# Performance work log

Measured on AMD Instinct MI355X. Metric: run time of the kernel, lower is better.

Reference implementation:

```python
import jax, jax.numpy as jnp
import numpy as np

P_PARTS = 6
NUM_CLASSES = 50000
BATCH = 128
PART_DIM = 256
LABEL_SMOOTH = 0.1
MARGIN = 0.3
TEMP = 3.0
KL_CLAMP = 5.0
LAMBDA_GRAPH = 0.1
LAMBDA_TRI = 1.0
LAMBDA_ADV = 0.1
START_EPOCH = 20


def setup_inputs() -> dict:
    key = jax.random.key(0)
    ks = jax.random.split(key, 8)
    id_logits = jax.random.normal(ks[0], (P_PARTS, BATCH, NUM_CLASSES), dtype=jnp.float32)
    id_features = jax.random.normal(ks[1], (P_PARTS, BATCH, PART_DIM), dtype=jnp.float32)
    gray_features = jax.random.normal(ks[2], (P_PARTS, BATCH, PART_DIM), dtype=jnp.float32)
    # soft labels are probability distributions (teacher softmax outputs)
    soft_labels = jax.nn.softmax(jax.random.normal(ks[3], (P_PARTS, BATCH, NUM_CLASSES), dtype=jnp.float32), axis=-1)
    entropy_weights = jax.random.uniform(ks[4], (P_PARTS, BATCH), dtype=jnp.float32)
    adv_logits = jax.random.normal(ks[5], (P_PARTS, BATCH, 2), dtype=jnp.float32)
    labels = jax.random.randint(ks[6], (BATCH,), 0, 16, dtype=jnp.int64 if jax.config.jax_enable_x64 else jnp.int32)
    modality_labels = jax.random.randint(ks[7], (BATCH,), 0, 2, dtype=jnp.int64 if jax.config.jax_enable_x64 else jnp.int32)
    return {
        'id_logits': id_logits,
        'id_features': id_features,
        'gray_features': gray_features,
        'soft_labels': soft_labels,
        'entropy_weights': entropy_weights,
        'adv_logits': adv_logits,
        'labels': labels,
        'modality_labels': modality_labels,
        'current_epoch': 25,
    }


def _ce(logits, labels, smoothing):
    # torch CrossEntropyLoss with label_smoothing, mean reduction. logits: [B,C]
    logp = jax.nn.log_softmax(logits, axis=-1)
    nll = -jnp.take_along_axis(logp, labels[:, None], axis=-1)[:, 0]
    smooth = -jnp.mean(logp, axis=-1)
    return jnp.mean((1.0 - smoothing) * nll + smoothing * smooth)


def _triplet(feat, target_feat, labels, same):
    # euclidean cdist [B,B]
    sq = (jnp.sum(feat * feat, axis=1)[:, None]
          + jnp.sum(target_feat * target_feat, axis=1)[None, :]
          - 2.0 * feat @ target_feat.T)
    dist = jnp.sqrt(jnp.clip(sq, 0.0) + 1e-12)
    eq = labels[:, None] == labels[None, :]
    is_neg = ~eq
    is_pos = eq & (~jnp.eye(feat.shape[0], dtype=bool)) if same else eq
    # vectorized hard mining (replaces per-row python loop)
    dist_ap = jnp.where(is_pos.any(axis=1),
                        jnp.max(jnp.where(is_pos, dist, -jnp.inf), axis=1), 0.0)
    dist_an = jnp.where(is_neg.any(axis=1),
                        jnp.min(jnp.where(is_neg, dist, jnp.inf), axis=1), 1e6)
    # MarginRankingLoss with y=1: mean(relu(dist_ap - dist_an + margin))
    return jnp.mean(jnp.maximum(dist_ap - dist_an + MARGIN, 0.0))


def reference(id_logits, id_features, gray_features, soft_labels, entropy_weights,
              adv_logits, labels, modality_labels, current_epoch):
    P = id_logits.shape[0]
    # --- multi-part ID loss ---
    L_id = jnp.mean(jax.vmap(lambda lg: _ce(lg, labels, LABEL_SMOOTH))(id_logits))
    # --- triplet on L2-normalized concatenated part features ---
    feat = jnp.concatenate(list(id_features), axis=1)  # [B, P*D]
    feat = feat / jnp.linalg.norm(feat, axis=1, keepdims=True)
    L_tri = _triplet(feat, feat, labels, same=True)
    feat_gray = jnp.concatenate(list(gray_features), axis=1)
    feat_gray = feat_gray / jnp.linalg.norm(feat_gray, axis=1, keepdims=True)
    L_trans = _triplet(feat, feat_gray, labels, same=False)
    L_tri = L_tri + 0.5 * L_trans
    # --- graph distillation (KL) ---
    if current_epoch >= START_EPOCH:
        logp = jax.nn.log_softmax(id_logits / TEMP, axis=-1)  # [P,B,C]
        kl = jnp.sum(soft_labels * (jnp.log(soft_labels) - logp), axis=-1)  # [P,B]
        kl = jnp.minimum(kl, KL_CLAMP)
        L_graph = jnp.sum(jnp.mean(kl * entropy_weights, axis=1)) * (TEMP ** 2) / P
    else:
        L_graph = jnp.float32(0.0)
    # --- adversarial CE ---
    logp_adv = jax.nn.log_softmax(adv_logits, axis=-1)  # [P,B,2]
    nll_adv = -jnp.take_along_axis(logp_adv, modality_labels[None, :, None], axis=-1)[..., 0]
    L_adv = jnp.mean(jnp.mean(nll_adv, axis=1))
    total = L_id + LAMBDA_TRI * L_tri + LAMBDA_GRAPH * L_graph + LAMBDA_ADV * L_adv
    return total
```

## Files before the change

### kernel.cpp

```cpp
#include <hip/hip_runtime.h>

#define NCLS   50000
#define NC4    12500
#define BATCH  128
#define PPARTS 6
#define NROWS  768
#define FD     1536

__device__ __forceinline__ float wave_sum(float v) {
#pragma unroll
  for (int off = 32; off > 0; off >>= 1) v += __shfl_xor(v, off, 64);
  return v;
}

__global__ void zero_k(float* acc) {
  if (threadIdx.x < 8) acc[threadIdx.x] = 0.0f;
}

__global__ __launch_bounds__(256) void big_rows_k(
    const float* __restrict__ X, const float* __restrict__ S,
    const float* __restrict__ W, const int* __restrict__ labels,
    float* __restrict__ acc) {
  const int row = blockIdx.x;
  const int b = row & (BATCH - 1);
  const int t = threadIdx.x;
  const size_t base = (size_t)row * NCLS;
  const float4* x4 = (const float4*)(X + base);
  const float4* s4 = (const float4*)(S + base);
  const float i3 = 1.0f / 3.0f;

  float x_lab = 0.0f;
  if (t == 0) x_lab = X[base + labels[b]];

  float m = -1e30f, e1 = 0.0f, e2 = 0.0f;
  float sx = 0.0f, ss = 0.0f, ssl = 0.0f, ssx = 0.0f;

  for (int i = t; i < NC4; i += 256) {
    float4 xv = x4[i];
    float4 sv = s4[i];
    float xs[4] = {xv.x, xv.y, xv.z, xv.w};
    float sc[4] = {sv.x, sv.y, sv.z, sv.w};
#pragma unroll
    for (int c = 0; c < 4; ++c) {
      float x = xs[c], s = sc[c];
      if (x > m) {
        float d = m - x;
        e1 *= __expf(d);
        e2 *= __expf(d * i3);
        m = x;
      }
      float d = x - m;
      e1 += __expf(d);
      e2 += __expf(d * i3);
      sx += x;
      ss += s;
      ssl = fmaf(s, __logf(s), ssl);
      ssx = fmaf(s, x, ssx);
    }
  }

#pragma unroll
  for (int off = 32; off > 0; off >>= 1) {
    float mo  = __shfl_xor(m, off, 64);
    float e1o = __shfl_xor(e1, off, 64);
    float e2o = __shfl_xor(e2, off, 64);
    float nm = fmaxf(m, mo);
    e1 = e1 * __expf(m - nm) + e1o * __expf(mo - nm);
    e2 = e2 * __expf((m - nm) * i3) + e2o * __expf((mo - nm) * i3);
    m = nm;
    sx  += __shfl_xor(sx, off, 64);
    ss  += __shfl_xor(ss, off, 64);
    ssl += __shfl_xor(ssl, off, 64);
    ssx += __shfl_xor(ssx, off, 64);
  }

  __shared__ float rm[4], re1[4], re2[4], rsx[4], rss[4], rssl[4], rssx[4];
  const int lane = t & 63, wid = t >> 6;
  if (lane == 0) {
    rm[wid] = m; re1[wid] = e1; re2[wid] = e2;
    rsx[wid] = sx; rss[wid] = ss; rssl[wid] = ssl; rssx[wid] = ssx;
  }
  __syncthreads();
  if (t == 0) {
    float M = rm[0], E1 = re1[0], E2 = re2[0];
#pragma unroll
    for (int wv = 1; wv < 4; ++wv) {
      float nm = fmaxf(M, rm[wv]);
      E1 = E1 * __expf(M - nm) + re1[wv] * __expf(rm[wv] - nm);
      E2 = E2 * __expf((M - nm) * i3) + re2[wv] * __expf((rm[wv] - nm) * i3);
      M = nm;
    }
    float SX  = rsx[0] + rsx[1] + rsx[2] + rsx[3];
    float SS  = rss[0] + rss[1] + rss[2] + rss[3];
    float SSL = rssl[0] + rssl[1] + rssl[2] + rssl[3];
    float SSX = rssx[0] + rssx[1] + rssx[2] + rssx[3];
    float logZ  = M + __logf(E1);
    float logZT = M * i3 + __logf(E2);
    float ce = 0.9f * (logZ - x_lab) + 0.1f * (logZ - SX * (1.0f / NCLS));
    float kl = SSL - SSX * i3 + logZT * SS;
    kl = fminf(kl, 5.0f);
    atomicAdd(&acc[0], ce);
    atomicAdd(&acc[1], kl * W[row]);
  }
}

__global__ __launch_bounds__(256) void normalize_k(
    const float* __restrict__ idf, const float* __restrict__ grayf,
    float* __restrict__ Fn, float* __restrict__ Gn) {
  const int src = blockIdx.x >> 7;
  const int b = blockIdx.x & (BATCH - 1);
  const int t = threadIdx.x;
  const float* in = src ? grayf : idf;
  float* out = src ? Gn : Fn;

  float v[6];
  float sq = 0.0f;
#pragma unroll
  for (int k = 0; k < 6; ++k) {
    v[k] = in[((k * BATCH + b) << 8) + t];
    sq = fmaf(v[k], v[k], sq);
  }
  sq = wave_sum(sq);
  __shared__ float wsum[4];
  __shared__ float inv_s;
  const int lane = t & 63, wid = t >> 6;
  if (lane == 0) wsum[wid] = sq;
  __syncthreads();
  if (t == 0) inv_s = 1.0f / sqrtf(wsum[0] + wsum[1] + wsum[2] + wsum[3]);
  __syncthreads();
  float inv = inv_s;
#pragma unroll
  for (int k = 0; k < 6; ++k)
    out[b * FD + (k << 8) + t] = v[k] * inv;
}

__global__ __launch_bounds__(256) void dist_k(
    const float* __restrict__ Fn, const float* __restrict__ Gn,
    float* __restrict__ D) {
  const int z = blockIdx.z;
  const float* Bm = z ? Gn : Fn;
  const int i0 = blockIdx.y * 16, j0 = blockIdx.x * 16;
  const int tx = threadIdx.x, ty = threadIdx.y;
  __shared__ float As[16][17], Bs[16][17];
  float acc = 0.0f;
  for (int k0 = 0; k0 < FD; k0 += 16) {
    As[ty][tx] = Fn[(i0 + ty) * FD + k0 + tx];
    Bs[ty][tx] = Bm[(j0 + ty) * FD + k0 + tx];
    __syncthreads();
#pragma unroll
    for (int k = 0; k < 16; ++k) acc = fmaf(As[ty][k], Bs[tx][k], acc);
    __syncthreads();
  }
  float sq = fmaxf(2.0f - 2.0f * acc, 0.0f) + 1e-12f;
  D[z * BATCH * BATCH + (i0 + ty) * BATCH + j0 + tx] = sqrtf(sq);
}

__global__ void mine_k(const float* __restrict__ D,
                       const int* __restrict__ labels, float* __restrict__ acc) {
  const int b = threadIdx.x;
  __shared__ int slab[BATCH];
  slab[b] = labels[b];
  __syncthreads();
  const int lb = slab[b];
  const float* d1 = D + b * BATCH;
  const float* d2 = D + BATCH * BATCH + b * BATCH;
  float ap1 = -1e30f, an1 = 1e30f, ap2 = -1e30f, an2 = 1e30f;
  int hasp1 = 0, hasn = 0, hasp2 = 0;
  for (int j = 0; j < BATCH; ++j) {
    bool eq = (slab[j] == lb);
    float v1 = d1[j], v2 = d2[j];
    if (eq) {
      hasp2 = 1; ap2 = fmaxf(ap2, v2);
      if (j != b) { hasp1 = 1; ap1 = fmaxf(ap1, v1); }
    } else {
      hasn = 1; an1 = fminf(an1, v1); an2 = fminf(an2, v2);
    }
  }
  float dap1 = hasp1 ? ap1 : 0.0f;
  float dan1 = hasn ? an1 : 1e6f;
  float l1 = fmaxf(dap1 - dan1 + 0.3f, 0.0f);
  float dap2 = hasp2 ? ap2 : 0.0f;
  float dan2 = hasn ? an2 : 1e6f;
  float l2 = fmaxf(dap2 - dan2 + 0.3f, 0.0f);
  l1 = wave_sum(l1);
  l2 = wave_sum(l2);
  __shared__ float r1[2], r2[2];
  const int lane = b & 63, wid = b >> 6;
  if (lane == 0) { r1[wid] = l1; r2[wid] = l2; }
  __syncthreads();
  if (b == 0) { acc[2] = r1[0] + r1[1]; acc[3] = r2[0] + r2[1]; }
}

__global__ void adv_k(const float* __restrict__ advl,
                      const int* __restrict__ mod, float* __restrict__ acc) {
  const int t = threadIdx.x;
  float sum = 0.0f;
#pragma unroll
  for (int k = 0; k < 3; ++k) {
    int r = t + k * 256;
    int b = r & (BATCH - 1);
    float l0 = advl[2 * r], l1 = advl[2 * r + 1];
    float mx = fmaxf(l0, l1);
    float lse = mx + __logf(__expf(l0 - mx) + __expf(l1 - mx));
    sum += lse - (mod[b] ? l1 : l0);
  }
  sum = wave_sum(sum);
  __shared__ float rs[4];
  const int lane = t & 63, wid = t >> 6;
  if (lane == 0) rs[wid] = sum;
  __syncthreads();
  if (t == 0) acc[4] = rs[0] + rs[1] + rs[2] + rs[3];
}

__global__ void fin_k(const float* __restrict__ acc,
                      const int* __restrict__ epoch, float* __restrict__ out) {
  float L_id = acc[0] * (1.0f / NROWS);
  float L_tri = acc[2] * (1.0f / BATCH) + 0.5f * acc[3] * (1.0f / BATCH);
  float L_graph = (epoch[0] >= 20) ? acc[1] * (9.0f / (6.0f * BATCH)) : 0.0f;
  float L_adv = acc[4] * (1.0f / NROWS);
  out[0] = L_id + 1.0f * L_tri + 0.1f * L_graph + 0.1f * L_adv;
}

extern "C" void kernel_launch(void* const* d_in, const int* in_sizes, int n_in,
                              void* d_out, int out_size, void* d_ws, size_t ws_size,
                              hipStream_t stream) {
  (void)in_sizes; (void)n_in; (void)out_size; (void)ws_size;
  const float* id_logits = (const float*)d_in[0];
  const float* id_feat   = (const float*)d_in[1];
  const float* gray_feat = (const float*)d_in[2];
  const float* soft      = (const float*)d_in[3];
  const float* entw      = (const float*)d_in[4];
  const float* advl      = (const float*)d_in[5];
  const int*   labels    = (const int*)d_in[6];
  const int*   modality  = (const int*)d_in[7];
  const int*   epoch     = (const int*)d_in[8];
  float* out = (float*)d_out;

  float* acc = (float*)d_ws;
  float* Fn  = acc + 16;
  float* Gn  = Fn + BATCH * FD;
  float* D   = Gn + BATCH * FD;

  zero_k<<<1, 64, 0, stream>>>(acc);
  big_rows_k<<<NROWS, 256, 0, stream>>>(id_logits, soft, entw, labels, acc);
  normalize_k<<<256, 256, 0, stream>>>(id_feat, gray_feat, Fn, Gn);
  dist_k<<<dim3(8, 8, 2), dim3(16, 16), 0, stream>>>(Fn, Gn, D);
  mine_k<<<1, BATCH, 0, stream>>>(D, labels, acc);
  adv_k<<<1, 256, 0, stream>>>(advl, modality, acc);
  fin_k<<<1, 1, 0, stream>>>(acc, epoch, out);
}
```

Baseline: 407.8 us.

## Restructure loss pipeline: fewer launches, chunked online softmax, fused tail kernel

The big row-reduction kernel now runs 512 threads per row and processes each float4 as a chunk, taking one max and one rescale per four elements instead of a per-element branch. Normalization now stores only inverse norms, which the distance GEMM applies directly to the raw features using 32x32 tiles with a 2x2 register block. Mining, the adversarial CE and finalization are fused into one tail kernel, and the accumulator zeroing moves into the norm kernel, cutting the launch count from seven to four. The main cost targeted is the memory-bound 768-row pass plus per-launch overhead; the risk is lower occupancy or register pressure at 512 threads.

```diff
diff --git a/kernel.cpp b/kernel.cpp
--- a/kernel.cpp
+++ b/kernel.cpp
@@ -13,11 +13,31 @@
   return v;
 }
 
-__global__ void zero_k(float* acc) {
-  if (threadIdx.x < 8) acc[threadIdx.x] = 0.0f;
-}
-
-__global__ __launch_bounds__(256) void big_rows_k(
+#define WS_INVF 16
+#define WS_INVG 144
+#define WS_D    272
+
+__device__ __forceinline__ void chunk_update(float4 xv, float4 sv,
+    float& m, float& e1, float& e2, float& sx, float& ss, float& ssl, float& ssx) {
+  const float i3 = 1.0f / 3.0f;
+  float cm = fmaxf(fmaxf(xv.x, xv.y), fmaxf(xv.z, xv.w));
+  float nm = fmaxf(m, cm);
+  float d0 = xv.x - nm, d1 = xv.y - nm, d2 = xv.z - nm, d3 = xv.w - nm;
+  float r = m - nm;
+  e1 = fmaf(e1, __expf(r),
+            (__expf(d0) + __expf(d1)) + (__expf(d2) + __expf(d3)));
+  e2 = fmaf(e2, __expf(r * i3),
+            (__expf(d0 * i3) + __expf(d1 * i3)) + (__expf(d2 * i3) + __expf(d3 * i3)));
+  m = nm;
+  sx += (xv.x + xv.y) + (xv.z + xv.w);
+  ss += (sv.x + sv.y) + (sv.z + sv.w);
+  ssl = fmaf(sv.x, __logf(sv.x), fmaf(sv.y, __logf(sv.y),
+        fmaf(sv.z, __logf(sv.z), fmaf(sv.w, __logf(sv.w), ssl))));
+  ssx = fmaf(sv.x, xv.x, fmaf(sv.y, xv.y,
+        fmaf(sv.z, xv.z, fmaf(sv.w, xv.w, ssx))));
+}
+
+__global__ __launch_bounds__(512) void big_rows_k(
     const float* __restrict__ X, const float* __restrict__ S,
     const float* __restrict__ W, const int* __restrict__ labels,
     float* __restrict__ acc) {
@@ -29,34 +49,19 @@
   const float4* s4 = (const float4*)(S + base);
   const float i3 = 1.0f / 3.0f;
 
-  float x_lab = 0.0f;
-  if (t == 0) x_lab = X[base + labels[b]];
+  float x_lab = (t == 0) ? X[base + labels[b]] : 0.0f;
 
   float m = -1e30f, e1 = 0.0f, e2 = 0.0f;
   float sx = 0.0f, ss = 0.0f, ssl = 0.0f, ssx = 0.0f;
 
-  for (int i = t; i < NC4; i += 256) {
-    float4 xv = x4[i];
-    float4 sv = s4[i];
-    float xs[4] = {xv.x, xv.y, xv.z, xv.w};
-    float sc[4] = {sv.x, sv.y, sv.z, sv.w};
-#pragma unroll
-    for (int c = 0; c < 4; ++c) {
-      float x = xs[c], s = sc[c];
-      if (x > m) {
-        float d = m - x;
-        e1 *= __expf(d);
-        e2 *= __expf(d * i3);
-        m = x;
-      }
-      float d = x - m;
-      e1 += __expf(d);
-      e2 += __expf(d * i3);
-      sx += x;
-      ss += s;
-      ssl = fmaf(s, __logf(s), ssl);
-      ssx = fmaf(s, x, ssx);
-    }
+#pragma unroll 4
+  for (int k = 0; k < 24; ++k) {
+    int i = t + (k << 9);
+    chunk_update(x4[i], s4[i], m, e1, e2, sx, ss, ssl, ssx);
+  }
+  {
+    int i = 12288 + t;
+    if (i < NC4) chunk_update(x4[i], s4[i], m, e1, e2, sx, ss, ssl, ssx);
   }
 
 #pragma unroll
@@ -74,7 +79,7 @@
     ssx += __shfl_xor(ssx, off, 64);
   }
 
-  __shared__ float rm[4], re1[4], re2[4], rsx[4], rss[4], rssl[4], rssx[4];
+  __shared__ float rm[8], re1[8], re2[8], rsx[8], rss[8], rssl[8], rssx[8];
   const int lane = t & 63, wid = t >> 6;
   if (lane == 0) {
     rm[wid] = m; re1[wid] = e1; re2[wid] = e2;
@@ -84,16 +89,15 @@
   if (t == 0) {
     float M = rm[0], E1 = re1[0], E2 = re2[0];
 #pragma unroll
-    for (int wv = 1; wv < 4; ++wv) {
+    for (int wv = 1; wv < 8; ++wv) {
       float nm = fmaxf(M, rm[wv]);
       E1 = E1 * __expf(M - nm) + re1[wv] * __expf(rm[wv] - nm);
       E2 = E2 * __expf((M - nm) * i3) + re2[wv] * __expf((rm[wv] - nm) * i3);
       M = nm;
     }
-    float SX  = rsx[0] + rsx[1] + rsx[2] + rsx[3];
-    float SS  = rss[0] + rss[1] + rss[2] + rss[3];
-    float SSL = rssl[0] + rssl[1] + rssl[2] + rssl[3];
-    float SSX = rssx[0] + rssx[1] + rssx[2] + rssx[3];
+    float SX = 0.f, SS = 0.f, SSL = 0.f, SSX = 0.f;
+#pragma unroll
+    for (int wv = 0; wv < 8; ++wv) { SX += rsx[wv]; SS += rss[wv]; SSL += rssl[wv]; SSX += rssx[wv]; }
     float logZ  = M + __logf(E1);
     float logZT = M * i3 + __logf(E2);
     float ce = 0.9f * (logZ - x_lab) + 0.1f * (logZ - SX * (1.0f / NCLS));
@@ -104,121 +108,129 @@
   }
 }
 
-__global__ __launch_bounds__(256) void normalize_k(
+__global__ __launch_bounds__(256) void norm_k(
     const float* __restrict__ idf, const float* __restrict__ grayf,
-    float* __restrict__ Fn, float* __restrict__ Gn) {
+    float* __restrict__ ws) {
   const int src = blockIdx.x >> 7;
   const int b = blockIdx.x & (BATCH - 1);
   const int t = threadIdx.x;
   const float* in = src ? grayf : idf;
-  float* out = src ? Gn : Fn;
-
-  float v[6];
   float sq = 0.0f;
 #pragma unroll
   for (int k = 0; k < 6; ++k) {
-    v[k] = in[((k * BATCH + b) << 8) + t];
-    sq = fmaf(v[k], v[k], sq);
+    float v = in[((k * BATCH + b) << 8) + t];
+    sq = fmaf(v, v, sq);
   }
   sq = wave_sum(sq);
-  __shared__ float wsum[4];
-  __shared__ float inv_s;
+  __shared__ float w4[4];
   const int lane = t & 63, wid = t >> 6;
-  if (lane == 0) wsum[wid] = sq;
-  __syncthreads();
-  if (t == 0) inv_s = 1.0f / sqrtf(wsum[0] + wsum[1] + wsum[2] + wsum[3]);
-  __syncthreads();
-  float inv = inv_s;
-#pragma unroll
-  for (int k = 0; k < 6; ++k)
-    out[b * FD + (k << 8) + t] = v[k] * inv;
+  if (lane == 0) w4[wid] = sq;
+  __syncthreads();
+  if (t == 0)
+    ws[16 + src * BATCH + b] = 1.0f / sqrtf(w4[0] + w4[1] + w4[2] + w4[3]);
+  if (blockIdx.x == 0 && t < 16) ws[t] = 0.0f;
 }
 
 __global__ __launch_bounds__(256) void dist_k(
-    const float* __restrict__ Fn, const float* __restrict__ Gn,
-    float* __restrict__ D) {
+    const float* __restrict__ idf, const float* __restrict__ grayf,
+    float* __restrict__ ws) {
   const int z = blockIdx.z;
-  const float* Bm = z ? Gn : Fn;
-  const int i0 = blockIdx.y * 16, j0 = blockIdx.x * 16;
-  const int tx = threadIdx.x, ty = threadIdx.y;
-  __shared__ float As[16][17], Bs[16][17];
-  float acc = 0.0f;
-  for (int k0 = 0; k0 < FD; k0 += 16) {
-    As[ty][tx] = Fn[(i0 + ty) * FD + k0 + tx];
-    Bs[ty][tx] = Bm[(j0 + ty) * FD + k0 + tx];
+  const float* Bm = z ? grayf : idf;
+  const float* invJsrc = ws + (z ? WS_INVG : WS_INVF);
+  const float* invIsrc = ws + WS_INVF;
+  float* D = ws + WS_D + z * BATCH * BATCH;
+  const int i0 = blockIdx.y * 32, j0 = blockIdx.x * 32;
+  const int t = threadIdx.x;
+
+  __shared__ float As[32][33], Bs[32][33];
+  __shared__ float sInvI[32], sInvJ[32];
+  if (t < 32) sInvI[t] = invIsrc[i0 + t];
+  else if (t < 64) sInvJ[t - 32] = invJsrc[j0 + t - 32];
+
+  const int lr = t >> 3, lk = (t & 7) << 2;
+  const int ty = t >> 4, tx = t & 15;
+
+  float c00 = 0.f, c01 = 0.f, c10 = 0.f, c11 = 0.f;
+  for (int k0 = 0; k0 < FD; k0 += 32) {
+    const int p = (k0 + lk) >> 8;
+    const int kin = (k0 + lk) & 255;
+    float4 av = *(const float4*)&idf[((p * BATCH + i0 + lr) << 8) + kin];
+    float4 bv = *(const float4*)&Bm [((p * BATCH + j0 + lr) << 8) + kin];
+    As[lr][lk] = av.x; As[lr][lk+1] = av.y; As[lr][lk+2] = av.z; As[lr][lk+3] = av.w;
+    Bs[lr][lk] = bv.x; Bs[lr][lk+1] = bv.y; Bs[lr][lk+2] = bv.z; Bs[lr][lk+3] = bv.w;
     __syncthreads();
 #pragma unroll
-    for (int k = 0; k < 16; ++k) acc = fmaf(As[ty][k], Bs[tx][k], acc);
+    for (int k = 0; k < 32; ++k) {
+      float a0 = As[2*ty][k],   a1 = As[2*ty+1][k];
+      float b0 = Bs[2*tx][k],   b1 = Bs[2*tx+1][k];
+      c00 = fmaf(a0, b0, c00);  c01 = fmaf(a0, b1, c01);
+      c10 = fmaf(a1, b0, c10);  c11 = fmaf(a1, b1, c11);
+    }
     __syncthreads();
   }
-  float sq = fmaxf(2.0f - 2.0f * acc, 0.0f) + 1e-12f;
-  D[z * BATCH * BATCH + (i0 + ty) * BATCH + j0 + tx] = sqrtf(sq);
-}
-
-__global__ void mine_k(const float* __restrict__ D,
-                       const int* __restrict__ labels, float* __restrict__ acc) {
-  const int b = threadIdx.x;
+  float ii0 = sInvI[2*ty], ii1 = sInvI[2*ty+1];
+  float jj0 = sInvJ[2*tx], jj1 = sInvJ[2*tx+1];
+  float g00 = c00*ii0*jj0, g01 = c01*ii0*jj1, g10 = c10*ii1*jj0, g11 = c11*ii1*jj1;
+  D[(i0+2*ty  )*BATCH + j0+2*tx  ] = sqrtf(fmaxf(2.f-2.f*g00, 0.f) + 1e-12f);
+  D[(i0+2*ty  )*BATCH + j0+2*tx+1] = sqrtf(fmaxf(2.f-2.f*g01, 0.f) + 1e-12f);
+  D[(i0+2*ty+1)*BATCH + j0+2*tx  ] = sqrtf(fmaxf(2.f-2.f*g10, 0.f) + 1e-12f);
+  D[(i0+2*ty+1)*BATCH + j0+2*tx+1] = sqrtf(fmaxf(2.f-2.f*g11, 0.f) + 1e-12f);
+}
+
+__global__ __launch_bounds__(256) void tail_k(
+    const float* __restrict__ ws_c, const float* __restrict__ advl,
+    const int* __restrict__ labels, const int* __restrict__ mod,
+    const int* __restrict__ epoch, float* __restrict__ out) {
+  const int t = threadIdx.x;
   __shared__ int slab[BATCH];
-  slab[b] = labels[b];
-  __syncthreads();
+  __shared__ float red[8];
+  if (t < BATCH) slab[t] = labels[t];
+  __syncthreads();
+
+  const int z = t >> 7;
+  const int b = t & (BATCH - 1);
   const int lb = slab[b];
-  const float* d1 = D + b * BATCH;
-  const float* d2 = D + BATCH * BATCH + b * BATCH;
-  float ap1 = -1e30f, an1 = 1e30f, ap2 = -1e30f, an2 = 1e30f;
-  int hasp1 = 0, hasn = 0, hasp2 = 0;
+  const float* drow = ws_c + WS_D + z * BATCH * BATCH + b * BATCH;
+  float ap = -1e30f, an = 1e30f;
+  int hasp = 0, hasn = 0;
+#pragma unroll 4
   for (int j = 0; j < BATCH; ++j) {
     bool eq = (slab[j] == lb);
-    float v1 = d1[j], v2 = d2[j];
-    if (eq) {
-      hasp2 = 1; ap2 = fmaxf(ap2, v2);
-      if (j != b) { hasp1 = 1; ap1 = fmaxf(ap1, v1); }
-    } else {
-      hasn = 1; an1 = fminf(an1, v1); an2 = fminf(an2, v2);
-    }
-  }
-  float dap1 = hasp1 ? ap1 : 0.0f;
-  float dan1 = hasn ? an1 : 1e6f;
-  float l1 = fmaxf(dap1 - dan1 + 0.3f, 0.0f);
-  float dap2 = hasp2 ? ap2 : 0.0f;
-  float dan2 = hasn ? an2 : 1e6f;
-  float l2 = fmaxf(dap2 - dan2 + 0.3f, 0.0f);
-  l1 = wave_sum(l1);
-  l2 = wave_sum(l2);
-  __shared__ float r1[2], r2[2];
-  const int lane = b & 63, wid = b >> 6;
-  if (lane == 0) { r1[wid] = l1; r2[wid] = l2; }
-  __syncthreads();
-  if (b == 0) { acc[2] = r1[0] + r1[1]; acc[3] = r2[0] + r2[1]; }
-}
-
-__global__ void adv_k(const float* __restrict__ advl,
-                      const int* __restrict__ mod, float* __restrict__ acc) {
-  const int t = threadIdx.x;
-  float sum = 0.0f;
+    float v = drow[j];
+    bool posok = eq && (z == 1 || j != b);
+    if (posok) { hasp = 1; ap = fmaxf(ap, v); }
+    if (!eq)   { hasn = 1; an = fminf(an, v); }
+  }
+  float dap = hasp ? ap : 0.0f;
+  float dan = hasn ? an : 1e6f;
+  float hinge = fmaxf(dap - dan + 0.3f, 0.0f);
+  hinge = wave_sum(hinge);
+
+  float advs = 0.0f;
 #pragma unroll
   for (int k = 0; k < 3; ++k) {
-    int r = t + k * 256;
-    int b = r & (BATCH - 1);
+    int r = t + (k << 8);
+    int rb = r & (BATCH - 1);
     float l0 = advl[2 * r], l1 = advl[2 * r + 1];
     float mx = fmaxf(l0, l1);
     float lse = mx + __logf(__expf(l0 - mx) + __expf(l1 - mx));
-    sum += lse - (mod[b] ? l1 : l0);
-  }
-  sum = wave_sum(sum);
-  __shared__ float rs[4];
+    advs += lse - (mod[rb] ? l1 : l0);
+  }
+  advs = wave_sum(advs);
+
   const int lane = t & 63, wid = t >> 6;
-  if (lane == 0) rs[wid] = sum;
-  __syncthreads();
-  if (t == 0) acc[4] = rs[0] + rs[1] + rs[2] + rs[3];
-}
-
-__global__ void fin_k(const float* __restrict__ acc,
-                      const int* __restrict__ epoch, float* __restrict__ out) {
-  float L_id = acc[0] * (1.0f / NROWS);
-  float L_tri = acc[2] * (1.0f / BATCH) + 0.5f * acc[3] * (1.0f / BATCH);
-  float L_graph = (epoch[0] >= 20) ? acc[1] * (9.0f / (6.0f * BATCH)) : 0.0f;
-  float L_adv = acc[4] * (1.0f / NROWS);
-  out[0] = L_id + 1.0f * L_tri + 0.1f * L_graph + 0.1f * L_adv;
+  if (lane == 0) { red[wid] = hinge; red[4 + wid] = advs; }
+  __syncthreads();
+  if (t == 0) {
+    float tri1 = red[0] + red[1];
+    float tri2 = red[2] + red[3];
+    float adv  = red[4] + red[5] + red[6] + red[7];
+    float L_id  = ws_c[0] * (1.0f / NROWS);
+    float L_tri = tri1 * (1.0f / BATCH) + 0.5f * tri2 * (1.0f / BATCH);
+    float L_graph = (epoch[0] >= 20) ? ws_c[1] * (9.0f / 768.0f) : 0.0f;
+    float L_adv = adv * (1.0f / NROWS);
+    out[0] = L_id + L_tri + 0.1f * L_graph + 0.1f * L_adv;
+  }
 }
 
 extern "C" void kernel_launch(void* const* d_in, const int* in_sizes, int n_in,
@@ -235,17 +247,10 @@
   const int*   modality  = (const int*)d_in[7];
   const int*   epoch     = (const int*)d_in[8];
   float* out = (float*)d_out;
-
-  float* acc = (float*)d_ws;
-  float* Fn  = acc + 16;
-  float* Gn  = Fn + BATCH * FD;
-  float* D   = Gn + BATCH * FD;
-
-  zero_k<<<1, 64, 0, stream>>>(acc);
-  big_rows_k<<<NROWS, 256, 0, stream>>>(id_logits, soft, entw, labels, acc);
-  normalize_k<<<256, 256, 0, stream>>>(id_feat, gray_feat, Fn, Gn);
-  dist_k<<<dim3(8, 8, 2), dim3(16, 16), 0, stream>>>(Fn, Gn, D);
-  mine_k<<<1, BATCH, 0, stream>>>(D, labels, acc);
-  adv_k<<<1, 256, 0, stream>>>(advl, modality, acc);
-  fin_k<<<1, 1, 0, stream>>>(acc, epoch, out);
-}
+  float* ws = (float*)d_ws;
+
+  norm_k<<<256, 256, 0, stream>>>(id_feat, gray_feat, ws);
+  dist_k<<<dim3(4, 4, 2), 256, 0, stream>>>(id_feat, gray_feat, ws);
+  big_rows_k<<<NROWS, 512, 0, stream>>>(id_logits, soft, entw, labels, ws);
+  tail_k<<<1, 256, 0, stream>>>(ws, advl, labels, modality, epoch, out);
+}
```

After: 411.4 us. About the same (+0.9%).
